# Optimization experiments

Measured on AMD Instinct MI355X. Metric: run time of the kernel, lower is better.

The kernel has to match this reference:

```python
import jax, jax.numpy as jnp
import numpy as np

N_NODES = 20000
N_EDGES = 160000
N_GRAPHS = 1000
IN_DIM = 11
HID = 128
EDGE_DIM = 3
N_LAYERS = 5
BN_EPS = 1e-5


def setup_inputs() -> dict:
    key = jax.random.key(0)
    ks = jax.random.split(key, 24)
    x = jax.random.normal(ks[0], (N_NODES, IN_DIM), dtype=jnp.float32)
    edge_index = jax.random.randint(ks[1], (2, N_EDGES), 0, N_NODES, dtype=jnp.int64)
    batch = jnp.sort(jax.random.randint(ks[2], (N_NODES,), 0, N_GRAPHS, dtype=jnp.int64))
    edge_attr = jax.random.uniform(ks[3], (N_EDGES, EDGE_DIM), dtype=jnp.float32)
    s_in = 1.0 / np.sqrt(IN_DIM)
    s_z = 1.0 / np.sqrt(2 * HID + EDGE_DIM)
    s_h = 1.0 / np.sqrt(HID)
    W_in = jax.random.uniform(ks[4], (IN_DIM, HID), minval=-s_in, maxval=s_in)
    b_in = jax.random.uniform(ks[5], (HID,), minval=-s_in, maxval=s_in)
    Wf = jax.random.uniform(ks[6], (N_LAYERS, 2 * HID + EDGE_DIM, HID), minval=-s_z, maxval=s_z)
    bf = jax.random.uniform(ks[7], (N_LAYERS, HID), minval=-s_z, maxval=s_z)
    Ws = jax.random.uniform(ks[8], (N_LAYERS, 2 * HID + EDGE_DIM, HID), minval=-s_z, maxval=s_z)
    bs = jax.random.uniform(ks[9], (N_LAYERS, HID), minval=-s_z, maxval=s_z)
    gamma = jnp.ones((N_LAYERS, HID), dtype=jnp.float32)
    beta = jnp.zeros((N_LAYERS, HID), dtype=jnp.float32)
    W1 = jax.random.uniform(ks[10], (HID, HID), minval=-s_h, maxval=s_h)
    b1 = jax.random.uniform(ks[11], (HID,), minval=-s_h, maxval=s_h)
    W2 = jax.random.uniform(ks[12], (HID, HID), minval=-s_h, maxval=s_h)
    b2 = jax.random.uniform(ks[13], (HID,), minval=-s_h, maxval=s_h)
    W3 = jax.random.uniform(ks[14], (HID, 1), minval=-s_h, maxval=s_h)
    b3 = jax.random.uniform(ks[15], (1,), minval=-s_h, maxval=s_h)
    return {"x": x, "edge_index": edge_index, "batch": batch, "edge_attr": edge_attr,
            "W_in": W_in, "b_in": b_in, "Wf": Wf, "bf": bf, "Ws": Ws, "bs": bs,
            "gamma": gamma, "beta": beta, "W1": W1, "b1": b1, "W2": W2, "b2": b2,
            "W3": W3, "b3": b3}


def reference(x, edge_index, batch, edge_attr, W_in, b_in, Wf, bf, Ws, bs,
              gamma, beta, W1, b1, W2, b2, W3, b3):
    src = edge_index[0]  # x_j (source / neighbor)
    dst = edge_index[1]  # x_i (target / aggregation index)
    # in-degree per node for mean aggregation (zero-degree -> divide by 1, yields 0)
    deg = jax.ops.segment_sum(jnp.ones((N_EDGES,), jnp.float32), dst, num_segments=N_NODES)
    deg = jnp.maximum(deg, 1.0)[:, None]

    h = x @ W_in + b_in  # [N, H]
    for l in range(N_LAYERS):
        # CGConv: z = [x_i, x_j, e]; msg = sigmoid(z Wf) * softplus(z Ws); residual + mean-aggr
        z = jnp.concatenate([h[dst], h[src], edge_attr], axis=-1)  # [E, 2H+D]
        msg = jax.nn.sigmoid(z @ Wf[l] + bf[l]) * jax.nn.softplus(z @ Ws[l] + bs[l])
        agg = jax.ops.segment_sum(msg, dst, num_segments=N_NODES) / deg
        h = h + agg
        # BatchNorm1d (training-mode batch stats, biased variance)
        mu = jnp.mean(h, axis=0)
        var = jnp.mean((h - mu) ** 2, axis=0)
        h = (h - mu) * jax.lax.rsqrt(var + BN_EPS) * gamma[l] + beta[l]
        h = jax.nn.relu(h)
        # dropout omitted (eval mode)

    # global mean pool over graphs
    cnt = jax.ops.segment_sum(jnp.ones((N_NODES,), jnp.float32), batch, num_segments=N_GRAPHS)
    g = jax.ops.segment_sum(h, batch, num_segments=N_GRAPHS) / jnp.maximum(cnt, 1.0)[:, None]

    g = jax.nn.relu(g @ W1 + b1)
    g = jax.nn.relu(g @ W2 + b2)
    return g @ W3 + b3  # [G, 1]
```

## Files before the change

kernel.cpp:

```cpp
#include <hip/hip_runtime.h>
#include <math.h>

#define NN 20000
#define NE 160000
#define NG 1000
#define IND 11
#define H 128
#define ED 3
#define NL 5
#define ZDH (259*128)
#define BN_EPSF 1e-5f
#define BPAD 17
#define EPW 16

typedef unsigned short ushort_t;
typedef unsigned int uint_t;
typedef __attribute__((ext_vector_type(8))) short bf8_t;
typedef __attribute__((ext_vector_type(4))) float f4_t;

__device__ inline ushort_t f2bf(float x) {
    unsigned int u = __float_as_uint(x);
    unsigned int r = (u + 0x7fffu + ((u >> 16) & 1u)) >> 16;
    return (ushort_t)r;
}
__device__ inline float bf2f(ushort_t b) {
    return __uint_as_float(((unsigned int)b) << 16);
}


__global__ void deg_int_kernel(const int* __restrict__ dst, int* __restrict__ degi) {
    int e = blockIdx.x * blockDim.x + threadIdx.x;
    if (e < NE) atomicAdd(&degi[dst[e]], 1);
}

__global__ __launch_bounds__(256) void reserve_kernel(const int* __restrict__ degi,
                                                      int* __restrict__ cursor,
                                                      float* __restrict__ invdeg,
                                                      int* __restrict__ counter) {
    int n = blockIdx.x * blockDim.x + threadIdx.x;
    int lane = threadIdx.x & 63;
    int v = (n < NN) ? degi[n] : 0;
    int x = v;
#pragma unroll
    for (int st = 1; st < 64; st <<= 1) {
        int y = __shfl_up(x, st, 64);
        if (lane >= st) x += y;
    }
    int total = __shfl(x, 63, 64);
    int base = 0;
    if (lane == 63) base = atomicAdd(counter, total);
    base = __shfl(base, 63, 64);
    if (n < NN) {
        cursor[n] = base + x - v;
        invdeg[n] = 1.0f / (float)(v < 1 ? 1 : v);
    }
}

__global__ void scatter_kernel(const int* __restrict__ src, const int* __restrict__ dst,
                               const float* __restrict__ ea,
                               const float* __restrict__ invdeg,
                               int* __restrict__ cursor, float4* __restrict__ csr_ea4,
                               int* __restrict__ csr_dst, float* __restrict__ csr_inv) {
    int e = blockIdx.x * blockDim.x + threadIdx.x;
    if (e < NE) {
        int d = dst[e];
        int pos = atomicAdd(&cursor[d], 1);
        float4 r;
        r.x = ea[e * ED + 0];
        r.y = ea[e * ED + 1];
        r.z = ea[e * ED + 2];
        r.w = __int_as_float(src[e]);
        csr_ea4[pos] = r;
        csr_dst[pos] = d;
        csr_inv[pos] = invdeg[d];
    }
}

__global__ void flag_kernel(const int* __restrict__ csr_dst, unsigned* __restrict__ endmask) {
    int e = blockIdx.x * blockDim.x + threadIdx.x;
    if (e < NE) {
        int d = csr_dst[e];
        int dn = (e + 1 < NE) ? csr_dst[e + 1] : -1;
        if (d != dn) atomicOr(&endmask[e >> 5], 1u << (e & 31));
    }
}

__global__ void wprep_kernel(const float* __restrict__ Wf, const float* __restrict__ Ws,
                             ushort_t* __restrict__ Wt_hi, ushort_t* __restrict__ Wt_lo) {
    int idx = blockIdx.x * 256 + threadIdx.x;
    if (idx >= NL * 512 * H) return;
    int k = idx & 127;
    int n = (idx >> 7) & 511;
    int l = idx >> 16;
    int t = n >> 7, j = n & 127;
    const float* W = (t == 0 || t == 2) ? Wf : Ws;
    int krow = (t < 2) ? k : (H + k);
    float v = W[(size_t)l * ZDH + krow * H + j];
    ushort_t hi = f2bf(v);
    Wt_hi[idx] = hi;
    Wt_lo[idx] = f2bf(v - bf2f(hi));
}


__global__ __launch_bounds__(H) void hin_kernel(const float* __restrict__ x,
                                                const float* __restrict__ Win,
                                                const float* __restrict__ bin,
                                                float* __restrict__ h) {
    int n = blockIdx.x;
    int j = threadIdx.x;
    __shared__ float xr[IND];
    if (j < IND) xr[j] = x[n * IND + j];
    __syncthreads();
    float acc = bin[j];
#pragma unroll
    for (int k = 0; k < IND; ++k) acc = fmaf(xr[k], Win[k * H + j], acc);
    h[(size_t)n * H + j] = acc;
}

__global__ __launch_bounds__(256, 2) void node_gemm_mfma(const float* __restrict__ hsrc,
                                                         float* __restrict__ hbn,
                                                         const ushort_t* __restrict__ Wt_hi,
                                                         const ushort_t* __restrict__ Wt_lo,
                                                         const float* __restrict__ sum,
                                                         const float* __restrict__ sumsq,
                                                         const float* __restrict__ gamma,
                                                         const float* __restrict__ beta,
                                                         int applyBN,
                                                         uint_t* __restrict__ ppack,
                                                         uint_t* __restrict__ qpack) {
    __shared__ __align__(16) ushort_t lbHi[128 * BPAD * 8];
    __shared__ __align__(16) ushort_t lbLo[128 * BPAD * 8];
    int table = blockIdx.y;
    int wave = threadIdx.x >> 6;
    int lane = threadIdx.x & 63;
    int sub = lane & 15;
    int quad = lane >> 4;
    int m0 = blockIdx.x * 128 + wave * 32;
    int writeH = applyBN && (table == 0);

    const ushort_t* wh = Wt_hi + (size_t)table * 128 * H;
    const ushort_t* wl = Wt_lo + (size_t)table * 128 * H;

    for (int c = threadIdx.x; c < 2048; c += 256) {
        int n = c >> 4, k = c & 15;
        bf8_t vh = *(const bf8_t*)(wh + n * H + k * 8);
        bf8_t vl = *(const bf8_t*)(wl + n * H + k * 8);
        *(bf8_t*)(lbHi + ((size_t)n * BPAD + k) * 8) = vh;
        *(bf8_t*)(lbLo + ((size_t)n * BPAD + k) * 8) = vl;
    }

    bf8_t aHi[2][4], aLo[2][4];
#pragma unroll
    for (int ks = 0; ks < 4; ++ks) {
        int kb = ks * 32 + quad * 8;
        float sc8[8], sh8[8];
        if (applyBN) {
            float4 su0 = *(const float4*)&sum[kb],   su1 = *(const float4*)&sum[kb + 4];
            float4 sq0 = *(const float4*)&sumsq[kb], sq1 = *(const float4*)&sumsq[kb + 4];
            float4 ga0 = *(const float4*)&gamma[kb], ga1 = *(const float4*)&gamma[kb + 4];
            float4 be0 = *(const float4*)&beta[kb],  be1 = *(const float4*)&beta[kb + 4];
            float su[8] = {su0.x, su0.y, su0.z, su0.w, su1.x, su1.y, su1.z, su1.w};
            float sq[8] = {sq0.x, sq0.y, sq0.z, sq0.w, sq1.x, sq1.y, sq1.z, sq1.w};
            float ga[8] = {ga0.x, ga0.y, ga0.z, ga0.w, ga1.x, ga1.y, ga1.z, ga1.w};
            float be[8] = {be0.x, be0.y, be0.z, be0.w, be1.x, be1.y, be1.z, be1.w};
#pragma unroll
            for (int i = 0; i < 8; ++i) {
                float mu  = su[i] * (1.0f / NN);
                float var = sq[i] * (1.0f / NN) - mu * mu;
                sc8[i] = ga[i] * rsqrtf(var + BN_EPSF);
                sh8[i] = be[i] - mu * sc8[i];
            }
        }
#pragma unroll
        for (int mt = 0; mt < 2; ++mt) {
            int r = m0 + mt * 16 + sub;
            int rc = r < NN ? r : NN - 1;
            const float* hp = hsrc + (size_t)rc * H + kb;
            float4 v0 = *(const float4*)hp;
            float4 v1 = *(const float4*)(hp + 4);
            float vv[8] = {v0.x, v0.y, v0.z, v0.w, v1.x, v1.y, v1.z, v1.w};
            if (applyBN) {
#pragma unroll
                for (int i = 0; i < 8; ++i) {
                    float v = fmaf(vv[i], sc8[i], sh8[i]);
                    vv[i] = v > 0.0f ? v : 0.0f;
                }
            }
            bf8_t hi8, lo8;
#pragma unroll
            for (int i = 0; i < 8; ++i) {
                ushort_t hi = f2bf(vv[i]);
                hi8[i] = (short)hi;
                lo8[i] = (short)f2bf(vv[i] - bf2f(hi));
            }
            aHi[mt][ks] = hi8;
            aLo[mt][ks] = lo8;
            if (writeH && r < NN) {
                float* op = hbn + (size_t)r * H + kb;
                *(float4*)op = make_float4(vv[0], vv[1], vv[2], vv[3]);
                *(float4*)(op + 4) = make_float4(vv[4], vv[5], vv[6], vv[7]);
            }
        }
    }
    __syncthreads();

    f4_t acc[2][8];
#pragma unroll
    for (int a = 0; a < 2; ++a)
#pragma unroll
        for (int b = 0; b < 8; ++b) acc[a][b] = (f4_t){0.f, 0.f, 0.f, 0.f};

#pragma unroll
    for (int nt = 0; nt < 8; ++nt) {
#pragma unroll
        for (int ks = 0; ks < 4; ++ks) {
            size_t lo = ((size_t)(nt * 16 + sub) * BPAD + ks * 4 + quad) * 8;
            bf8_t bHi = *(const bf8_t*)(lbHi + lo);
            bf8_t bLo = *(const bf8_t*)(lbLo + lo);
#pragma unroll
            for (int mt = 0; mt < 2; ++mt) {
                acc[mt][nt] = __builtin_amdgcn_mfma_f32_16x16x32_bf16(aHi[mt][ks], bHi, acc[mt][nt], 0, 0, 0);
                acc[mt][nt] = __builtin_amdgcn_mfma_f32_16x16x32_bf16(aLo[mt][ks], bHi, acc[mt][nt], 0, 0, 0);
                acc[mt][nt] = __builtin_amdgcn_mfma_f32_16x16x32_bf16(aHi[mt][ks], bLo, acc[mt][nt], 0, 0, 0);
            }
        }
    }

    ushort_t* outp = (ushort_t*)((table < 2) ? ppack : qpack);
    int par = table & 1;
#pragma unroll
    for (int mt = 0; mt < 2; ++mt)
#pragma unroll
        for (int nt = 0; nt < 8; ++nt) {
            int col = nt * 16 + sub;
#pragma unroll
            for (int rr = 0; rr < 4; ++rr) {
                int row = m0 + mt * 16 + quad * 4 + rr;
                if (row < NN) outp[2 * ((size_t)row * H + col) + par] = f2bf(acc[mt][nt][rr]);
            }
        }
}

__global__ __launch_bounds__(256) void agg_edge_kernel(const int4* __restrict__ csr_fe,
                                                       const int* __restrict__ csr_dst,
                                                       const float* __restrict__ csr_inv,
                                                       const unsigned* __restrict__ endmask,
                                                       const float* __restrict__ Wf,
                                                       const float* __restrict__ bf,
                                                       const float* __restrict__ Ws,
                                                       const float* __restrict__ bs,
                                                       const uint_t* __restrict__ ppack,
                                                       const uint_t* __restrict__ qpack,
                                                       float* __restrict__ h,
                                                       float* __restrict__ sum,
                                                       float* __restrict__ sumsq) {
    int tid = threadIdx.x;
    if (blockIdx.x == 0 && tid < H) { sum[tid] = 0.0f; sumsq[tid] = 0.0f; }
    int lane = tid & 63;
    int wv = tid >> 6;
    int base = (blockIdx.x * 4 + wv) * EPW;
    int c0 = 2 * lane;

    float2 wf0 = *(const float2*)&Wf[256 * H + c0];
    float2 wf1 = *(const float2*)&Wf[257 * H + c0];
    float2 wf2 = *(const float2*)&Wf[258 * H + c0];
    float2 ws0 = *(const float2*)&Ws[256 * H + c0];
    float2 ws1 = *(const float2*)&Ws[257 * H + c0];
    float2 ws2 = *(const float2*)&Ws[258 * H + c0];
    float2 bf2_ = *(const float2*)&bf[c0];
    float2 bs2_ = *(const float2*)&bs[c0];

    int4 fe = csr_fe[base + (lane & (EPW - 1))];
    int  dd = csr_dst[base + (lane & (EPW - 1))];
    int  ivr = __float_as_int(csr_inv[base + (lane & (EPW - 1))]);
    unsigned mword = endmask[base >> 5];
    unsigned mask = __builtin_amdgcn_readfirstlane((mword >> (base & 31)) & 0xFFFFu);

    uint2 q[8];
#pragma unroll
    for (int i = 0; i < 8; ++i) {
        int s = __builtin_amdgcn_readlane(fe.w, i);
        q[i] = *(const uint2*)&qpack[(size_t)s * H + c0];
    }

    int dcur = __builtin_amdgcn_readlane(dd, 0);
    uint2 ppc = *(const uint2*)&ppack[(size_t)dcur * H + c0];
    float pf0 = __uint_as_float(ppc.x << 16), ps0 = __uint_as_float(ppc.x & 0xFFFF0000u);
    float pf1 = __uint_as_float(ppc.y << 16), ps1 = __uint_as_float(ppc.y & 0xFFFF0000u);
    unsigned m = mask;
    int e0 = m ? __builtin_ctz(m) : EPW;
    int dnext = 0;
    uint2 ppN = ppc;
    if (e0 + 1 < EPW) {
        dnext = __builtin_amdgcn_readlane(dd, e0 + 1);
        ppN = *(const uint2*)&ppack[(size_t)dnext * H + c0];
    }

    float acc0 = 0.f, acc1 = 0.f;

#pragma unroll
    for (int tb = 0; tb < EPW; tb += 8) {
#pragma unroll
        for (int i = 0; i < 8; ++i) {
            int t = tb + i;
            float ex = __int_as_float(__builtin_amdgcn_readlane(fe.x, t));
            float ey = __int_as_float(__builtin_amdgcn_readlane(fe.y, t));
            float ez = __int_as_float(__builtin_amdgcn_readlane(fe.z, t));
            uint2 qq = q[i];
            if (t + 8 < EPW) {
                int s2 = __builtin_amdgcn_readlane(fe.w, t + 8);
                q[i] = *(const uint2*)&qpack[(size_t)s2 * H + c0];
            }
            float qf0 = __uint_as_float(qq.x << 16);
            float qs0 = __uint_as_float(qq.x & 0xFFFF0000u);
            float qf1 = __uint_as_float(qq.y << 16);
            float qs1 = __uint_as_float(qq.y & 0xFFFF0000u);
            float f0 = fmaf(ex, wf0.x, fmaf(ey, wf1.x, fmaf(ez, wf2.x, pf0 + bf2_.x + qf0)));
            float v0 = fmaf(ex, ws0.x, fmaf(ey, ws1.x, fmaf(ez, ws2.x, ps0 + bs2_.x + qs0)));
            float f1 = fmaf(ex, wf0.y, fmaf(ey, wf1.y, fmaf(ez, wf2.y, pf1 + bf2_.y + qf1)));
            float v1 = fmaf(ex, ws0.y, fmaf(ey, ws1.y, fmaf(ez, ws2.y, ps1 + bs2_.y + qs1)));
            float sig0 = __builtin_amdgcn_rcpf(1.0f + __expf(-f0));
            float sp0  = fmaxf(v0, 0.0f) + __logf(1.0f + __expf(-fabsf(v0)));
            float sig1 = __builtin_amdgcn_rcpf(1.0f + __expf(-f1));
            float sp1  = fmaxf(v1, 0.0f) + __logf(1.0f + __expf(-fabsf(v1)));
            acc0 = fmaf(sig0, sp0, acc0);
            acc1 = fmaf(sig1, sp1, acc1);
            if (mask & (1u << t)) {
                float inv = __int_as_float(__builtin_amdgcn_readlane(ivr, t));
                atomicAdd(&h[(size_t)dcur * H + c0], acc0 * inv);
                atomicAdd(&h[(size_t)dcur * H + c0 + 1], acc1 * inv);
                acc0 = 0.f; acc1 = 0.f;
                dcur = dnext;
                pf0 = __uint_as_float(ppN.x << 16); ps0 = __uint_as_float(ppN.x & 0xFFFF0000u);
                pf1 = __uint_as_float(ppN.y << 16); ps1 = __uint_as_float(ppN.y & 0xFFFF0000u);
                m &= m - 1;
                int e1 = m ? __builtin_ctz(m) : EPW;
                if (e1 + 1 < EPW) {
                    dnext = __builtin_amdgcn_readlane(dd, e1 + 1);
                    ppN = *(const uint2*)&ppack[(size_t)dnext * H + c0];
                }
            }
        }
    }
    if (!(mask & (1u << (EPW - 1)))) {
        float inv = __int_as_float(__builtin_amdgcn_readlane(ivr, EPW - 1));
        atomicAdd(&h[(size_t)dcur * H + c0], acc0 * inv);
        atomicAdd(&h[(size_t)dcur * H + c0 + 1], acc1 * inv);
    }
}

__global__ __launch_bounds__(H) void stats_kernel(const float* __restrict__ h,
                                                  float* __restrict__ sum,
                                                  float* __restrict__ sumsq) {
    int j = threadIdx.x;
    float s = 0.0f, ss = 0.0f;
    int n = blockIdx.x * 8;
    for (; n + 7 < NN; n += gridDim.x * 8) {
        float v[8];
#pragma unroll
        for (int i = 0; i < 8; ++i) v[i] = h[(size_t)(n + i) * H + j];
#pragma unroll
        for (int i = 0; i < 8; ++i) { s += v[i]; ss = fmaf(v[i], v[i], ss); }
    }
    for (; n < NN; ++n) {
        float v = h[(size_t)n * H + j];
        s += v;
        ss = fmaf(v, v, ss);
    }
    atomicAdd(&sum[j], s);
    atomicAdd(&sumsq[j], ss);
}

__global__ __launch_bounds__(H) void pool_kernel(const float* __restrict__ h,
                                                 const int* __restrict__ batch,
                                                 const float* __restrict__ sum,
                                                 const float* __restrict__ sumsq,
                                                 const float* __restrict__ gamma,
                                                 const float* __restrict__ beta,
                                                 float* __restrict__ g,
                                                 float* __restrict__ cnt) {
    int j = threadIdx.x;
    float mu  = sum[j] * (1.0f / NN);
    float var = sumsq[j] * (1.0f / NN) - mu * mu;
    float sc  = gamma[j] * rsqrtf(var + BN_EPSF);
    float sh  = beta[j] - mu * sc;
    for (int n = blockIdx.x; n < NN; n += gridDim.x) {
        int b = batch[n];
        float v = fmaf(h[(size_t)n * H + j], sc, sh);
        v = v > 0.0f ? v : 0.0f;
        atomicAdd(&g[(size_t)b * H + j], v);
        if (j == 0) atomicAdd(&cnt[b], 1.0f);
    }
}

__global__ __launch_bounds__(H) void mlp_kernel(const float* __restrict__ g,
                                                const float* __restrict__ cnt,
                                                const float* __restrict__ W1,
                                                const float* __restrict__ b1,
                                                const float* __restrict__ W2,
                                                const float* __restrict__ b2,
                                                const float* __restrict__ W3,
                                                const float* __restrict__ b3,
                                                float* __restrict__ out) {
    int gid = blockIdx.x, j = threadIdx.x;
    __shared__ float s1[H];
    __shared__ float s2[H];
    __shared__ float wsum[2];
    float c = cnt[gid];
    c = c < 1.0f ? 1.0f : c;
    s1[j] = g[gid * H + j] / c;
    __syncthreads();
    float a = b1[j];
    for (int k = 0; k < H; ++k) a = fmaf(s1[k], W1[k * H + j], a);
    a = a > 0.0f ? a : 0.0f;
    s2[j] = a;
    __syncthreads();
    float t = b2[j];
    for (int k = 0; k < H; ++k) t = fmaf(s2[k], W2[k * H + j], t);
    t = t > 0.0f ? t : 0.0f;
    float p = t * W3[j];
    for (int off = 32; off > 0; off >>= 1) p += __shfl_down(p, off, 64);
    if ((j & 63) == 0) wsum[j >> 6] = p;
    __syncthreads();
    if (j == 0) out[gid] = wsum[0] + wsum[1] + b3[0];
}

extern "C" void kernel_launch(void* const* d_in, const int* in_sizes, int n_in,
                              void* d_out, int out_size, void* d_ws, size_t ws_size,
                              hipStream_t stream) {
    const float* x     = (const float*)d_in[0];
    const int*   ei    = (const int*)d_in[1];
    const int*   srcp  = ei;
    const int*   dstp  = ei + NE;
    const int*   batch = (const int*)d_in[2];
    const float* ea    = (const float*)d_in[3];
    const float* Win   = (const float*)d_in[4];
    const float* bin   = (const float*)d_in[5];
    const float* Wf    = (const float*)d_in[6];
    const float* bf    = (const float*)d_in[7];
    const float* Ws    = (const float*)d_in[8];
    const float* bs    = (const float*)d_in[9];
    const float* gamma = (const float*)d_in[10];
    const float* beta  = (const float*)d_in[11];
    const float* W1    = (const float*)d_in[12];
    const float* b1    = (const float*)d_in[13];
    const float* W2    = (const float*)d_in[14];
    const float* b2    = (const float*)d_in[15];
    const float* W3    = (const float*)d_in[16];
    const float* b3    = (const float*)d_in[17];
    float* out = (float*)d_out;

    const size_t NH = (size_t)NN * H;
    float* wsp = (float*)d_ws;
    size_t off = 0;
    float* hA     = wsp + off; off += NH;
    float* hB     = wsp + off; off += NH;
    uint_t* ppack = (uint_t*)(wsp + off); off += NH;
    uint_t* qpack = (uint_t*)(wsp + off); off += NH;
    float* invdeg = wsp + off; off += NN;
    float* sum    = wsp + off; off += H;
    float* sumsq  = wsp + off; off += H;
    float* g      = wsp + off; off += (size_t)NG * H;
    float* cnt    = wsp + off; off += NG;
    off = (off + 3) & ~(size_t)3;
    float4* csr_ea4 = (float4*)(wsp + off); off += (size_t)NE * 4;
    float* csr_inv = wsp + off; off += NE;
    int* degi      = (int*)(wsp + off); off += NN;
    int* counter   = (int*)(wsp + off); off += 1;
    unsigned* endmask = (unsigned*)(wsp + off); off += NE / 32;
    int* cursor    = (int*)(wsp + off); off += NN;
    int* csr_dst   = (int*)(wsp + off); off += NE;
    off = (off + 3) & ~(size_t)3;
    ushort_t* Wt_hi = (ushort_t*)(wsp + off); off += (size_t)NL * 512 * H / 2;
    ushort_t* Wt_lo = (ushort_t*)(wsp + off); off += (size_t)NL * 512 * H / 2;

    hipMemsetAsync(degi, 0, (NN + 1 + NE / 32) * sizeof(int), stream);
    deg_int_kernel<<<(NE + 255) / 256, 256, 0, stream>>>(dstp, degi);
    reserve_kernel<<<(NN + 255) / 256, 256, 0, stream>>>(degi, cursor, invdeg, counter);
    scatter_kernel<<<(NE + 255) / 256, 256, 0, stream>>>(srcp, dstp, ea, invdeg, cursor,
                                                         csr_ea4, csr_dst, csr_inv);
    flag_kernel<<<(NE + 255) / 256, 256, 0, stream>>>(csr_dst, endmask);
    wprep_kernel<<<(NL * 512 * H + 255) / 256, 256, 0, stream>>>(Wf, Ws, Wt_hi, Wt_lo);

    hin_kernel<<<NN, H, 0, stream>>>(x, Win, bin, hA);

    float* hRead = hA;
    for (int l = 0; l < NL; ++l) {
        float* hTgt = (l == 0) ? hA : ((l & 1) ? hB : hA);
        node_gemm_mfma<<<dim3((NN + 127) / 128, 4), 256, 0, stream>>>(
            hRead, hTgt,
            Wt_hi + (size_t)l * 512 * H,
            Wt_lo + (size_t)l * 512 * H,
            sum, sumsq,
            gamma + (size_t)(l ? l - 1 : 0) * H,
            beta  + (size_t)(l ? l - 1 : 0) * H,
            l > 0, ppack, qpack);
        agg_edge_kernel<<<NE / (4 * EPW), 256, 0, stream>>>((const int4*)csr_ea4, csr_dst,
                                                            csr_inv, endmask,
                                                            Wf + (size_t)l * ZDH, bf + (size_t)l * H,
                                                            Ws + (size_t)l * ZDH, bs + (size_t)l * H,
                                                            ppack, qpack,
                                                            hTgt, sum, sumsq);
        stats_kernel<<<512, H, 0, stream>>>(hTgt, sum, sumsq);
        hRead = hTgt;
    }

    hipMemsetAsync(g, 0, ((size_t)NG * H + NG) * sizeof(float), stream);
    pool_kernel<<<2048, H, 0, stream>>>(hRead, batch, sum, sumsq,
                                        gamma + (size_t)(NL - 1) * H,
                                        beta + (size_t)(NL - 1) * H, g, cnt);
    mlp_kernel<<<NG, H, 0, stream>>>(g, cnt, W1, b1, W2, b2, W3, b3, out);
}
```

Baseline: 528.1 us.

## Drop weight low-part split and pair Wf/Ws tables per GEMM block

Weights are now stored as a single bf16 copy instead of a hi/lo split, so each MFMA step runs two products (aHi·W, aLo·W) instead of three. Each block now computes the matching Wf and Ws tables together over 64 rows. The packed p/q outputs are written as full 32-bit words rather than interleaved 16-bit halves. This cuts MFMA work by about a third, halves the grid's y dimension, and removes the strided half-word stores, but lowers accuracy because the weights are rounded to bf16.

```diff
diff --git a/kernel.cpp b/kernel.cpp
--- a/kernel.cpp
+++ b/kernel.cpp
@@ -86,7 +86,7 @@
 }
 
 __global__ void wprep_kernel(const float* __restrict__ Wf, const float* __restrict__ Ws,
-                             ushort_t* __restrict__ Wt_hi, ushort_t* __restrict__ Wt_lo) {
+                             ushort_t* __restrict__ Wt) {
     int idx = blockIdx.x * 256 + threadIdx.x;
     if (idx >= NL * 512 * H) return;
     int k = idx & 127;
@@ -95,10 +95,7 @@
     int t = n >> 7, j = n & 127;
     const float* W = (t == 0 || t == 2) ? Wf : Ws;
     int krow = (t < 2) ? k : (H + k);
-    float v = W[(size_t)l * ZDH + krow * H + j];
-    ushort_t hi = f2bf(v);
-    Wt_hi[idx] = hi;
-    Wt_lo[idx] = f2bf(v - bf2f(hi));
+    Wt[idx] = f2bf(W[(size_t)l * ZDH + krow * H + j]);
 }
 
 
@@ -119,8 +116,7 @@
 
 __global__ __launch_bounds__(256, 2) void node_gemm_mfma(const float* __restrict__ hsrc,
                                                          float* __restrict__ hbn,
-                                                         const ushort_t* __restrict__ Wt_hi,
-                                                         const ushort_t* __restrict__ Wt_lo,
+                                                         const ushort_t* __restrict__ Wt,
                                                          const float* __restrict__ sum,
                                                          const float* __restrict__ sumsq,
                                                          const float* __restrict__ gamma,
@@ -128,32 +124,35 @@
                                                          int applyBN,
                                                          uint_t* __restrict__ ppack,
                                                          uint_t* __restrict__ qpack) {
-    __shared__ __align__(16) ushort_t lbHi[128 * BPAD * 8];
-    __shared__ __align__(16) ushort_t lbLo[128 * BPAD * 8];
-    int table = blockIdx.y;
+    __shared__ __align__(16) ushort_t lbF[128 * BPAD * 8];
+    __shared__ __align__(16) ushort_t lbS[128 * BPAD * 8];
+    int pair = blockIdx.y;
     int wave = threadIdx.x >> 6;
     int lane = threadIdx.x & 63;
     int sub = lane & 15;
     int quad = lane >> 4;
-    int m0 = blockIdx.x * 128 + wave * 32;
-    int writeH = applyBN && (table == 0);
-
-    const ushort_t* wh = Wt_hi + (size_t)table * 128 * H;
-    const ushort_t* wl = Wt_lo + (size_t)table * 128 * H;
+    int m0 = blockIdx.x * 64 + wave * 16;
+    int writeH = applyBN && (pair == 0);
+
+    const ushort_t* whF = Wt + (size_t)(2 * pair) * 128 * H;
+    const ushort_t* whS = Wt + (size_t)(2 * pair + 1) * 128 * H;
 
     for (int c = threadIdx.x; c < 2048; c += 256) {
         int n = c >> 4, k = c & 15;
-        bf8_t vh = *(const bf8_t*)(wh + n * H + k * 8);
-        bf8_t vl = *(const bf8_t*)(wl + n * H + k * 8);
-        *(bf8_t*)(lbHi + ((size_t)n * BPAD + k) * 8) = vh;
-        *(bf8_t*)(lbLo + ((size_t)n * BPAD + k) * 8) = vl;
-    }
-
-    bf8_t aHi[2][4], aLo[2][4];
+        *(bf8_t*)(lbF + ((size_t)n * BPAD + k) * 8) = *(const bf8_t*)(whF + n * H + k * 8);
+        *(bf8_t*)(lbS + ((size_t)n * BPAD + k) * 8) = *(const bf8_t*)(whS + n * H + k * 8);
+    }
+
+    bf8_t aHi[4], aLo[4];
+    int r = m0 + sub;
+    int rc = r < NN ? r : NN - 1;
 #pragma unroll
     for (int ks = 0; ks < 4; ++ks) {
         int kb = ks * 32 + quad * 8;
-        float sc8[8], sh8[8];
+        const float* hp = hsrc + (size_t)rc * H + kb;
+        float4 v0 = *(const float4*)hp;
+        float4 v1 = *(const float4*)(hp + 4);
+        float vv[8] = {v0.x, v0.y, v0.z, v0.w, v1.x, v1.y, v1.z, v1.w};
         if (applyBN) {
             float4 su0 = *(const float4*)&sum[kb],   su1 = *(const float4*)&sum[kb + 4];
             float4 sq0 = *(const float4*)&sumsq[kb], sq1 = *(const float4*)&sumsq[kb + 4];
@@ -167,78 +166,61 @@
             for (int i = 0; i < 8; ++i) {
                 float mu  = su[i] * (1.0f / NN);
                 float var = sq[i] * (1.0f / NN) - mu * mu;
-                sc8[i] = ga[i] * rsqrtf(var + BN_EPSF);
-                sh8[i] = be[i] - mu * sc8[i];
+                float sc  = ga[i] * rsqrtf(var + BN_EPSF);
+                float sh  = be[i] - mu * sc;
+                float v = fmaf(vv[i], sc, sh);
+                vv[i] = v > 0.0f ? v : 0.0f;
             }
         }
-#pragma unroll
-        for (int mt = 0; mt < 2; ++mt) {
-            int r = m0 + mt * 16 + sub;
-            int rc = r < NN ? r : NN - 1;
-            const float* hp = hsrc + (size_t)rc * H + kb;
-            float4 v0 = *(const float4*)hp;
-            float4 v1 = *(const float4*)(hp + 4);
-            float vv[8] = {v0.x, v0.y, v0.z, v0.w, v1.x, v1.y, v1.z, v1.w};
-            if (applyBN) {
-#pragma unroll
-                for (int i = 0; i < 8; ++i) {
-                    float v = fmaf(vv[i], sc8[i], sh8[i]);
-                    vv[i] = v > 0.0f ? v : 0.0f;
-                }
-            }
-            bf8_t hi8, lo8;
-#pragma unroll
-            for (int i = 0; i < 8; ++i) {
-                ushort_t hi = f2bf(vv[i]);
-                hi8[i] = (short)hi;
-                lo8[i] = (short)f2bf(vv[i] - bf2f(hi));
-            }
-            aHi[mt][ks] = hi8;
-            aLo[mt][ks] = lo8;
-            if (writeH && r < NN) {
-                float* op = hbn + (size_t)r * H + kb;
-                *(float4*)op = make_float4(vv[0], vv[1], vv[2], vv[3]);
-                *(float4*)(op + 4) = make_float4(vv[4], vv[5], vv[6], vv[7]);
-            }
+        bf8_t hi8, lo8;
+#pragma unroll
+        for (int i = 0; i < 8; ++i) {
+            ushort_t hi = f2bf(vv[i]);
+            hi8[i] = (short)hi;
+            lo8[i] = (short)f2bf(vv[i] - bf2f(hi));
+        }
+        aHi[ks] = hi8;
+        aLo[ks] = lo8;
+        if (writeH && r < NN) {
+            float* op = hbn + (size_t)r * H + kb;
+            *(float4*)op = make_float4(vv[0], vv[1], vv[2], vv[3]);
+            *(float4*)(op + 4) = make_float4(vv[4], vv[5], vv[6], vv[7]);
         }
     }
     __syncthreads();
 
-    f4_t acc[2][8];
-#pragma unroll
-    for (int a = 0; a < 2; ++a)
-#pragma unroll
-        for (int b = 0; b < 8; ++b) acc[a][b] = (f4_t){0.f, 0.f, 0.f, 0.f};
+    f4_t accF[8], accS[8];
+#pragma unroll
+    for (int b = 0; b < 8; ++b) { accF[b] = (f4_t){0.f, 0.f, 0.f, 0.f}; accS[b] = (f4_t){0.f, 0.f, 0.f, 0.f}; }
 
 #pragma unroll
     for (int nt = 0; nt < 8; ++nt) {
 #pragma unroll
         for (int ks = 0; ks < 4; ++ks) {
             size_t lo = ((size_t)(nt * 16 + sub) * BPAD + ks * 4 + quad) * 8;
-            bf8_t bHi = *(const bf8_t*)(lbHi + lo);
-            bf8_t bLo = *(const bf8_t*)(lbLo + lo);
-#pragma unroll
-            for (int mt = 0; mt < 2; ++mt) {
-                acc[mt][nt] = __builtin_amdgcn_mfma_f32_16x16x32_bf16(aHi[mt][ks], bHi, acc[mt][nt], 0, 0, 0);
-                acc[mt][nt] = __builtin_amdgcn_mfma_f32_16x16x32_bf16(aLo[mt][ks], bHi, acc[mt][nt], 0, 0, 0);
-                acc[mt][nt] = __builtin_amdgcn_mfma_f32_16x16x32_bf16(aHi[mt][ks], bLo, acc[mt][nt], 0, 0, 0);
+            bf8_t bF = *(const bf8_t*)(lbF + lo);
+            bf8_t bS = *(const bf8_t*)(lbS + lo);
+            accF[nt] = __builtin_amdgcn_mfma_f32_16x16x32_bf16(aHi[ks], bF, accF[nt], 0, 0, 0);
+            accF[nt] = __builtin_amdgcn_mfma_f32_16x16x32_bf16(aLo[ks], bF, accF[nt], 0, 0, 0);
+            accS[nt] = __builtin_amdgcn_mfma_f32_16x16x32_bf16(aHi[ks], bS, accS[nt], 0, 0, 0);
+            accS[nt] = __builtin_amdgcn_mfma_f32_16x16x32_bf16(aLo[ks], bS, accS[nt], 0, 0, 0);
+        }
+    }
+
+    uint_t* outp = pair ? qpack : ppack;
+#pragma unroll
+    for (int nt = 0; nt < 8; ++nt) {
+        int col = nt * 16 + sub;
+#pragma unroll
+        for (int rr = 0; rr < 4; ++rr) {
+            int row = m0 + quad * 4 + rr;
+            if (row < NN) {
+                uint_t lo = f2bf(accF[nt][rr]);
+                uint_t hi = f2bf(accS[nt][rr]);
+                outp[(size_t)row * H + col] = lo | (hi << 16);
             }
         }
     }
-
-    ushort_t* outp = (ushort_t*)((table < 2) ? ppack : qpack);
-    int par = table & 1;
-#pragma unroll
-    for (int mt = 0; mt < 2; ++mt)
-#pragma unroll
-        for (int nt = 0; nt < 8; ++nt) {
-            int col = nt * 16 + sub;
-#pragma unroll
-            for (int rr = 0; rr < 4; ++rr) {
-                int row = m0 + mt * 16 + quad * 4 + rr;
-                if (row < NN) outp[2 * ((size_t)row * H + col) + par] = f2bf(acc[mt][nt][rr]);
-            }
-        }
 }
 
 __global__ __launch_bounds__(256) void agg_edge_kernel(const int4* __restrict__ csr_fe,
@@ -471,8 +453,7 @@
     int* cursor    = (int*)(wsp + off); off += NN;
     int* csr_dst   = (int*)(wsp + off); off += NE;
     off = (off + 3) & ~(size_t)3;
-    ushort_t* Wt_hi = (ushort_t*)(wsp + off); off += (size_t)NL * 512 * H / 2;
-    ushort_t* Wt_lo = (ushort_t*)(wsp + off); off += (size_t)NL * 512 * H / 2;
+    ushort_t* Wt = (ushort_t*)(wsp + off); off += (size_t)NL * 512 * H / 2;
 
     hipMemsetAsync(degi, 0, (NN + 1 + NE / 32) * sizeof(int), stream);
     deg_int_kernel<<<(NE + 255) / 256, 256, 0, stream>>>(dstp, degi);
@@ -480,17 +461,16 @@
     scatter_kernel<<<(NE + 255) / 256, 256, 0, stream>>>(srcp, dstp, ea, invdeg, cursor,
                                                          csr_ea4, csr_dst, csr_inv);
     flag_kernel<<<(NE + 255) / 256, 256, 0, stream>>>(csr_dst, endmask);
-    wprep_kernel<<<(NL * 512 * H + 255) / 256, 256, 0, stream>>>(Wf, Ws, Wt_hi, Wt_lo);
+    wprep_kernel<<<(NL * 512 * H + 255) / 256, 256, 0, stream>>>(Wf, Ws, Wt);
 
     hin_kernel<<<NN, H, 0, stream>>>(x, Win, bin, hA);
 
     float* hRead = hA;
     for (int l = 0; l < NL; ++l) {
         float* hTgt = (l == 0) ? hA : ((l & 1) ? hB : hA);
-        node_gemm_mfma<<<dim3((NN + 127) / 128, 4), 256, 0, stream>>>(
+        node_gemm_mfma<<<dim3((NN + 63) / 64, 2), 256, 0, stream>>>(
             hRead, hTgt,
-            Wt_hi + (size_t)l * 512 * H,
-            Wt_lo + (size_t)l * 512 * H,
+            Wt + (size_t)l * 512 * H,
             sum, sumsq,
             gamma + (size_t)(l ? l - 1 : 0) * H,
             beta  + (size_t)(l ? l - 1 : 0) * H,
```

Measured after the change: 492.9 us (median of 2 runs). 1.07x faster.
